# Optimization experiments

Measured on AMD Instinct MI355X. Metric: run time of the kernel, lower is better.

The kernel has to match this reference:

```python
import jax, jax.numpy as jnp
import numpy as np

MONOTONICITY = 1.0  # init kwarg monotonicity=1


def _interp_channel(xq, xs, ys):
    """Monotonic piecewise-linear interp for one channel.
    xq: (N,) query points; xs: (B,) sorted breakpoints; ys: (B,) knot values.
    Linear extrapolation beyond both ends using the edge segment slopes.
    """
    B = xs.shape[0]
    # segment index in [1, B-1]; elements below xs[0] / above xs[-1] use edge segments
    idx = jnp.clip(jnp.searchsorted(xs, xq), 1, B - 1)
    x0 = xs[idx - 1]
    x1 = xs[idx]
    y0 = ys[idx - 1]
    y1 = ys[idx]
    slope = (y1 - y0) / (x1 - x0)
    return y0 + slope * (xq - x0)


def setup_inputs() -> dict:
    key = jax.random.key(0)
    k1, k2, k3, k4 = jax.random.split(key, 4)
    N, C, B = 2097152, 16, 32
    x = jax.random.normal(k1, (N, C), dtype=jnp.float32)
    # learned parameters of MonoPointPWL (per channel)
    xp = jax.random.normal(k2, (C, B), dtype=jnp.float32)        # raw x positions (sorted at use)
    y0 = jax.random.normal(k3, (C,), dtype=jnp.float32)          # y value at first knot
    dy = jax.random.normal(k4, (C, B - 1), dtype=jnp.float32)    # raw segment deltas
    return {"x": x, "xp": xp, "y0": y0, "dy": dy}


def reference(x, xp, y0, dy):
    # sorted breakpoint x positions per channel: (C, B)
    xs = jnp.sort(xp, axis=1)
    # monotone knot values: y0 + cumsum(|dy|) * monotonicity, (C, B)
    steps = jnp.abs(dy) * MONOTONICITY
    ys = y0[:, None] + jnp.concatenate(
        [jnp.zeros_like(y0)[:, None], jnp.cumsum(steps, axis=1)], axis=1
    )
    # vectorize over channels: x is (N, C), params are (C, B)
    out = jax.vmap(_interp_channel, in_axes=(1, 0, 0), out_axes=1)(x, xs, ys)
    return out
```

## Files before the change

kernel.cpp:

```cpp
#include <hip/hip_runtime.h>
#include <hip/hip_bf16.h>


#define C_CH 16
#define B_KN 32

__global__ __launch_bounds__(512) void pwl_setup_kernel(
    const float* __restrict__ xp, const float* __restrict__ y0,
    const float* __restrict__ dy, float* __restrict__ ws) {
    __shared__ float s_x[C_CH][B_KN];
    __shared__ float s_xs[C_CH][B_KN];
    __shared__ float s_ys[C_CH][B_KN];
    int t = threadIdx.x;
    int c = t >> 5;
    int k = t & 31;
    float v = xp[c * B_KN + k];
    s_x[c][k] = v;
    __syncthreads();
    int rank = 0;
#pragma unroll
    for (int j = 0; j < B_KN; ++j) {
        float u = s_x[c][j];
        rank += (u < v || (u == v && j < k)) ? 1 : 0;
    }
    s_xs[c][rank] = v;
    float acc = y0[c];
    for (int j = 0; j < k; ++j) acc += fabsf(dy[c * (B_KN - 1) + j]);
    s_ys[c][k] = acc;
    __syncthreads();
    ws[c * B_KN + k] = s_xs[c][k];
    if (k < B_KN - 1) {
        float x0 = s_xs[c][k], x1 = s_xs[c][k + 1];
        float ya = s_ys[c][k], yb = s_ys[c][k + 1];
        float a = (yb - ya) / (x1 - x0);
        float b = ya - a * x0;
        ws[512 + c * B_KN + k]  = a;
        ws[1024 + c * B_KN + k] = b;
    }
}

__global__ __launch_bounds__(256) void pwl_main_kernel(
    const float4* __restrict__ x, float4* __restrict__ out,
    const float* __restrict__ ws, int n4) {
    __shared__ float s_xs[C_CH][B_KN + 1];
    __shared__ float s_a[C_CH][B_KN];
    __shared__ float s_b[C_CH][B_KN];
    for (int i = threadIdx.x; i < C_CH * B_KN; i += 256) {
        int c = i >> 5, k = i & 31;
        s_xs[c][k] = ws[i];
        s_a[c][k]  = ws[512 + i];
        s_b[c][k]  = ws[1024 + i];
    }
    __syncthreads();

    int tid = blockIdx.x * 256 + threadIdx.x;
    int stride = gridDim.x * 256;
    for (int i = tid; i < n4; i += stride) {
        float4 v = x[i];
        int c0 = (i & 3) << 2;
        float xv[4] = {v.x, v.y, v.z, v.w};
        float r[4];
#pragma unroll
        for (int j = 0; j < 4; ++j) {
            int c = c0 + j;
            float xq = xv[j];
            const float* xs = s_xs[c];
            int pos = 0;
#pragma unroll
            for (int s = 16; s >= 1; s >>= 1)
                pos += (xs[pos + s - 1] < xq) ? s : 0;
            int seg = (pos > 1 ? pos : 1) - 1;
            r[j] = fmaf(s_a[c][seg], xq, s_b[c][seg]);
        }
        out[i] = make_float4(r[0], r[1], r[2], r[3]);
    }
}

extern "C" void kernel_launch(void* const* d_in, const int* in_sizes, int n_in,
                              void* d_out, int out_size, void* d_ws, size_t ws_size,
                              hipStream_t stream) {
    const float* x  = (const float*)d_in[0];
    const float* xp = (const float*)d_in[1];
    const float* y0 = (const float*)d_in[2];
    const float* dy = (const float*)d_in[3];
    float* out = (float*)d_out;
    float* ws  = (float*)d_ws;

    pwl_setup_kernel<<<1, 512, 0, stream>>>(xp, y0, dy, ws);

    int n4 = in_sizes[0] / 4;
    int blocks = (n4 + 255) / 256;
    if (blocks > 2048) blocks = 2048;
    pwl_main_kernel<<<blocks, 256, 0, stream>>>((const float4*)x, (float4*)out, ws, n4);
}
```

Before: 52.66 us.

## Replace binary search with per-channel quantized bucket LUT plus short linear scan

Adds a kernel that builds, for each channel, a 512-bucket lookup table over [-6,6] holding the range of breakpoint indices that can fall inside each bucket. The main kernel turns each query into a bucket index, reads the LUT from shared memory and scans only the few candidate breakpoints, replacing the 5-step dependent binary search. It also packs the slope and intercept into a float2 and software-prefetches the next float4 of input. The costs are an extra kernel launch, more shared memory per block (which may lower occupancy), and a data-dependent scan loop that can diverge.

```diff
diff --git a/kernel.cpp b/kernel.cpp
--- a/kernel.cpp
+++ b/kernel.cpp
@@ -4,6 +4,12 @@
 
 #define C_CH 16
 #define B_KN 32
+#define QB 512
+#define LUT_S 528
+#define LO_F (-6.0f)
+#define STEP_F (12.0f / QB)
+#define INVSTEP_F (QB / 12.0f)
+
 
 __global__ __launch_bounds__(512) void pwl_setup_kernel(
     const float* __restrict__ xp, const float* __restrict__ y0,
@@ -39,40 +45,74 @@
     }
 }
 
+__global__ __launch_bounds__(256) void pwl_lut_kernel(
+    const float* __restrict__ ws, unsigned short* __restrict__ lut) {
+    int idx = blockIdx.x * 256 + threadIdx.x;
+    if (idx >= C_CH * QB) return;
+    int c = idx >> 9;
+    int q = idx & (QB - 1);
+    const float* xs = ws + c * B_KN;
+    float lo = LO_F + q * STEP_F;
+    float hi = lo + STEP_F;
+    int p0 = 0, p1 = 0;
+#pragma unroll
+    for (int j = 0; j < B_KN; ++j) {
+        float v = xs[j];
+        p0 += (q > 0 && v < lo) ? 1 : 0;
+        p1 += (q == QB - 1 || v < hi) ? 1 : 0;
+    }
+    lut[idx] = (unsigned short)(p0 | (p1 << 8));
+}
+
 __global__ __launch_bounds__(256) void pwl_main_kernel(
     const float4* __restrict__ x, float4* __restrict__ out,
     const float* __restrict__ ws, int n4) {
-    __shared__ float s_xs[C_CH][B_KN + 1];
-    __shared__ float s_a[C_CH][B_KN];
-    __shared__ float s_b[C_CH][B_KN];
+    __shared__ float  s_xs[C_CH][B_KN + 1];
+    __shared__ float2 s_ab[C_CH][B_KN + 1];
+    __shared__ unsigned short s_lut[C_CH][LUT_S];
     for (int i = threadIdx.x; i < C_CH * B_KN; i += 256) {
         int c = i >> 5, k = i & 31;
         s_xs[c][k] = ws[i];
-        s_a[c][k]  = ws[512 + i];
-        s_b[c][k]  = ws[1024 + i];
+        s_ab[c][k] = make_float2(ws[512 + i], ws[1024 + i]);
+    }
+    const unsigned short* lut_g = (const unsigned short*)(ws + 1536);
+    for (int i = threadIdx.x; i < C_CH * QB; i += 256) {
+        s_lut[i >> 9][i & (QB - 1)] = lut_g[i];
     }
     __syncthreads();
 
     int tid = blockIdx.x * 256 + threadIdx.x;
     int stride = gridDim.x * 256;
-    for (int i = tid; i < n4; i += stride) {
-        float4 v = x[i];
-        int c0 = (i & 3) << 2;
+    int c0 = (threadIdx.x & 3) << 2;
+    int i = tid;
+    if (i >= n4) return;
+    float4 v = x[i];
+    while (true) {
+        int inext = i + stride;
+        float4 vn = v;
+        if (inext < n4) vn = x[inext];
         float xv[4] = {v.x, v.y, v.z, v.w};
         float r[4];
 #pragma unroll
         for (int j = 0; j < 4; ++j) {
             int c = c0 + j;
             float xq = xv[j];
-            const float* xs = s_xs[c];
-            int pos = 0;
-#pragma unroll
-            for (int s = 16; s >= 1; s >>= 1)
-                pos += (xs[pos + s - 1] < xq) ? s : 0;
-            int seg = (pos > 1 ? pos : 1) - 1;
-            r[j] = fmaf(s_a[c][seg], xq, s_b[c][seg]);
+            int q = (int)((xq - LO_F) * INVSTEP_F);
+            q = q < 0 ? 0 : (q > QB - 1 ? QB - 1 : q);
+            int lv = s_lut[c][q];
+            int p0 = lv & 63;
+            int p1 = lv >> 8;
+            int pos = p0;
+            for (int t = p0; t < p1; ++t)
+                pos += (s_xs[c][t] < xq) ? 1 : 0;
+            int seg = pos < 2 ? 0 : (pos > 31 ? 30 : pos - 1);
+            float2 ab = s_ab[c][seg];
+            r[j] = fmaf(ab.x, xq, ab.y);
         }
         out[i] = make_float4(r[0], r[1], r[2], r[3]);
+        if (inext >= n4) break;
+        i = inext;
+        v = vn;
     }
 }
 
@@ -87,6 +127,8 @@
     float* ws  = (float*)d_ws;
 
     pwl_setup_kernel<<<1, 512, 0, stream>>>(xp, y0, dy, ws);
+    pwl_lut_kernel<<<(C_CH * QB + 255) / 256, 256, 0, stream>>>(
+        ws, (unsigned short*)(ws + 1536));
 
     int n4 = in_sizes[0] / 4;
     int blocks = (n4 + 255) / 256;
```

Result: slower. 70.75 us (+34.4%).

## Bank-replicate lookup tables in LDS, register top search levels, prefetch next float4

Applied to the files above, without the earlier changes.

Each channel's breakpoint and coefficient tables are replicated 32 times across LDS banks, so every lane reads its own bank. This removes LDS bank conflicts in the binary search. The first three search levels come from values held in registers, and only the last two levels plus the coefficient fetch touch LDS. The grid-stride loop software-prefetches the next float4, and the launch becomes 768 blocks of 512 threads. The cost is 48KB of LDS per block and a larger table-fill prologue in every block.

```diff
diff --git a/kernel.cpp b/kernel.cpp
--- a/kernel.cpp
+++ b/kernel.cpp
@@ -4,6 +4,8 @@
 
 #define C_CH 16
 #define B_KN 32
+#define TAB_WORDS 12288
+
 
 __global__ __launch_bounds__(512) void pwl_setup_kernel(
     const float* __restrict__ xp, const float* __restrict__ y0,
@@ -36,43 +38,79 @@
         float b = ya - a * x0;
         ws[512 + c * B_KN + k]  = a;
         ws[1024 + c * B_KN + k] = b;
+    } else {
+        ws[512 + c * B_KN + k]  = 0.0f;
+        ws[1024 + c * B_KN + k] = 0.0f;
     }
 }
 
-__global__ __launch_bounds__(256) void pwl_main_kernel(
+__global__ __launch_bounds__(512, 6) void pwl_main_kernel(
     const float4* __restrict__ x, float4* __restrict__ out,
     const float* __restrict__ ws, int n4) {
-    __shared__ float s_xs[C_CH][B_KN + 1];
-    __shared__ float s_a[C_CH][B_KN];
-    __shared__ float s_b[C_CH][B_KN];
-    for (int i = threadIdx.x; i < C_CH * B_KN; i += 256) {
-        int c = i >> 5, k = i & 31;
-        s_xs[c][k] = ws[i];
-        s_a[c][k]  = ws[512 + i];
-        s_b[c][k]  = ws[1024 + i];
+    __shared__ float s_tab[TAB_WORDS];
+    int t = threadIdx.x;
+    for (int w = t; w < TAB_WORDS; w += 512) {
+        int bk = w & 31;
+        int r  = w >> 5;
+        int m  = r / 96;
+        int tt = r - m * 96;
+        int arr = tt >> 5;
+        int idx = tt & 31;
+        int c = ((bk & 3) << 2) + m;
+        s_tab[w] = ws[arr * 512 + c * 32 + idx];
+    }
+    int c0 = (t & 3) << 2;
+    float v15[4], v7[4], v23[4], v3[4], v11[4], v19[4], v27[4];
+#pragma unroll
+    for (int j = 0; j < 4; ++j) {
+        const float* xs = ws + (c0 + j) * B_KN;
+        v15[j] = xs[15];
+        v7[j]  = xs[7];
+        v23[j] = xs[23];
+        v3[j]  = xs[3];
+        v11[j] = xs[11];
+        v19[j] = xs[19];
+        v27[j] = xs[27];
     }
     __syncthreads();
 
-    int tid = blockIdx.x * 256 + threadIdx.x;
-    int stride = gridDim.x * 256;
-    for (int i = tid; i < n4; i += stride) {
-        float4 v = x[i];
-        int c0 = (i & 3) << 2;
+    int bk = t & 31;
+    int tid = blockIdx.x * 512 + t;
+    int stride = gridDim.x * 512;
+
+    int i = tid;
+    if (i >= n4) return;
+    float4 v = x[i];
+    while (true) {
+        int inext = i + stride;
+        float4 vn = v;
+        if (inext < n4) vn = x[inext];
         float xv[4] = {v.x, v.y, v.z, v.w};
         float r[4];
 #pragma unroll
         for (int j = 0; j < 4; ++j) {
-            int c = c0 + j;
             float xq = xv[j];
-            const float* xs = s_xs[c];
-            int pos = 0;
-#pragma unroll
-            for (int s = 16; s >= 1; s >>= 1)
-                pos += (xs[pos + s - 1] < xq) ? s : 0;
-            int seg = (pos > 1 ? pos : 1) - 1;
-            r[j] = fmaf(s_a[c][seg], xq, s_b[c][seg]);
+            bool b16 = (v15[j] < xq);
+            float l2v = b16 ? v23[j] : v7[j];
+            bool b8 = (l2v < xq);
+            float l3a = b16 ? v19[j] : v3[j];
+            float l3b = b16 ? v27[j] : v11[j];
+            float l3v = b8 ? l3b : l3a;
+            bool b4 = (l3v < xq);
+            int pos = (b16 ? 16 : 0) + (b8 ? 8 : 0) + (b4 ? 4 : 0);
+            float w1 = s_tab[((j * 96 + (pos + 1)) << 5) | bk];
+            pos += (w1 < xq) ? 2 : 0;
+            float w2 = s_tab[((j * 96 + pos) << 5) | bk];
+            pos += (w2 < xq) ? 1 : 0;
+            int seg = pos < 2 ? 0 : (pos > 31 ? 30 : pos - 1);
+            float a = s_tab[((j * 96 + 32 + seg) << 5) | bk];
+            float b = s_tab[((j * 96 + 64 + seg) << 5) | bk];
+            r[j] = fmaf(a, xq, b);
         }
         out[i] = make_float4(r[0], r[1], r[2], r[3]);
+        if (inext >= n4) break;
+        i = inext;
+        v = vn;
     }
 }
 
@@ -89,7 +127,6 @@
     pwl_setup_kernel<<<1, 512, 0, stream>>>(xp, y0, dy, ws);
 
     int n4 = in_sizes[0] / 4;
-    int blocks = (n4 + 255) / 256;
-    if (blocks > 2048) blocks = 2048;
-    pwl_main_kernel<<<blocks, 256, 0, stream>>>((const float4*)x, (float4*)out, ws, n4);
+    int blocks = 768;
+    pwl_main_kernel<<<blocks, 512, 0, stream>>>((const float4*)x, (float4*)out, ws, n4);
 }
```

New measurement: 57.86 us. +9.9%, slower.
